# Kernel tuning notes

Hardware: AMD Instinct MI355X
Metric: run time of the kernel (lower is better)

The kernel has to match this reference:

```python
import jax, jax.numpy as jnp
import numpy as np

N_QUBITS = 10
N_LAYERS = 4
DIM = 2 ** N_QUBITS


def _bit(v, q, n):
    return (v >> (n - 1 - q)) & 1


def _cnot_indices(control, target, n):
    idx0, idx1 = [], []
    for i in range(2 ** n):
        if _bit(i, control, n) == 1 and _bit(i, target, n) == 0:
            idx0.append(i)
            idx1.append(i | (1 << (n - 1 - target)))
    return np.asarray(idx0, np.int32), np.asarray(idx1, np.int32)


# static precomputed CNOT swap indices for pairs (q, (q+1) % n)
_CNOT = [_cnot_indices(q, (q + 1) % N_QUBITS, N_QUBITS) for q in range(N_QUBITS)]
# Z expectation masks: [n_qubits, dim] of +/-1
_ZMASK = np.array([[1.0 - 2.0 * _bit(i, q, N_QUBITS) for i in range(DIM)]
                   for q in range(N_QUBITS)], np.float32)


def _rx(t):
    c = jnp.cos(t / 2.0).astype(jnp.complex64)
    s = jnp.sin(t / 2.0).astype(jnp.complex64)
    return jnp.stack([jnp.stack([c, -1j * s], -1),
                      jnp.stack([-1j * s, c], -1)], -2)


def _ry(t):
    c = jnp.cos(t / 2.0).astype(jnp.complex64)
    s = jnp.sin(t / 2.0).astype(jnp.complex64)
    return jnp.stack([jnp.stack([c, -s], -1),
                      jnp.stack([s, c], -1)], -2)


def _rz(t):
    tc = t.astype(jnp.complex64)
    e0 = jnp.exp(-1j * tc / 2.0)
    e1 = jnp.exp(1j * tc / 2.0)
    z = jnp.zeros_like(e0)
    return jnp.stack([jnp.stack([e0, z], -1),
                      jnp.stack([z, e1], -1)], -2)


def _apply_gate(state, gate, q):
    # state: [b, DIM] complex64; gate: [2,2] or [b,2,2]
    b = state.shape[0]
    psi = state.reshape((b,) + (2,) * N_QUBITS)
    psi = jnp.moveaxis(psi, q + 1, N_QUBITS).reshape(b, DIM // 2, 2)
    if gate.ndim == 3:
        out = jnp.einsum('bmi,bij->bmj', psi, gate)
    else:
        out = jnp.einsum('bmi,ij->bmj', psi, gate)
    out = out.reshape((b,) + (2,) * N_QUBITS)
    out = jnp.moveaxis(out, N_QUBITS, q + 1)
    return out.reshape(b, DIM)


def _cnot(state, idx0, idx1):
    return state.at[:, idx0].set(state[:, idx1]).at[:, idx1].set(state[:, idx0])


def setup_inputs() -> dict:
    key = jax.random.key(0)
    k1, k2, k3, k4 = jax.random.split(key, 4)
    x = jax.random.normal(k1, (16384, 3), jnp.float32)
    enc_W = jax.random.normal(k2, (N_QUBITS, 3), jnp.float32) * 0.3
    enc_b = jax.random.normal(k3, (N_QUBITS,), jnp.float32) * 0.1
    theta = jax.random.normal(k4, (N_LAYERS, N_QUBITS, 3), jnp.float32) * 0.04
    return {"x": x, "enc_W": enc_W, "enc_b": enc_b, "theta": theta}


def reference(x, enc_W, enc_b, theta):
    b = x.shape[0]
    enc = jnp.pi * jnp.tanh(x @ enc_W.T + enc_b)  # [b, n_qubits]
    state = jnp.zeros((b, DIM), jnp.complex64).at[:, 0].set(1.0 + 0j)
    # batched encoding RY rotations
    for q in range(N_QUBITS):
        state = _apply_gate(state, _ry(enc[:, q]), q)
    # variational layers (shared gate across batch)
    for layer in range(N_LAYERS):
        for q in range(N_QUBITS):
            state = _apply_gate(state, _rx(theta[layer, q, 0]), q)
            state = _apply_gate(state, _ry(theta[layer, q, 1]), q)
            state = _apply_gate(state, _rz(theta[layer, q, 2]), q)
        for idx0, idx1 in _CNOT:
            state = _cnot(state, idx0, idx1)
    probs = jnp.square(state.real) + jnp.square(state.imag)  # [b, DIM]
    return probs @ jnp.asarray(_ZMASK).T  # [b, n_qubits]
```

## Files before the change

kernel.cpp:

```cpp
#include <hip/hip_runtime.h>
#include <stdint.h>

#define NQ 10
#define NL 4

typedef unsigned int u32;
typedef _Float16 f16x8 __attribute__((ext_vector_type(8)));
typedef float f32x16 __attribute__((ext_vector_type(16)));
typedef u32 u32x4 __attribute__((ext_vector_type(4)));


__device__ __forceinline__ f32x16 mfma16(f16x8 a, f16x8 b, f32x16 c) {
    return __builtin_amdgcn_mfma_f32_32x32x16_f16(a, b, c, 0, 0, 0);
}
__device__ __forceinline__ f32x16 zero16() {
    f32x16 z;
#pragma unroll
    for (int i = 0; i < 16; i++) z[i] = 0.f;
    return z;
}
__device__ __forceinline__ f16x8 negf(f16x8 v) {
    u32x4 u = __builtin_bit_cast(u32x4, v);
#pragma unroll
    for (int i = 0; i < 4; i++) u[i] ^= 0x80008000u;
    return __builtin_bit_cast(f16x8, u);
}
__device__ __forceinline__ u32 pk2(float a, float b) {
    auto h = __builtin_amdgcn_cvt_pkrtz(a, b);
    return __builtin_bit_cast(u32, h);
}
__device__ __forceinline__ u32 mixhl(u32 s, u32 x) {
    return __builtin_amdgcn_perm(s, x, 0x07060100u);
}
__device__ __forceinline__ f16x8 mk8(u32 a, u32 b, u32 c, u32 d) {
    u32x4 v; v[0] = a; v[1] = b; v[2] = c; v[3] = d;
    return __builtin_bit_cast(f16x8, v);
}
template <int MASK>
__device__ __forceinline__ float swz(float v) {
    return __int_as_float(__builtin_amdgcn_ds_swizzle(__float_as_int(v), (MASK << 10) | 0x1F));
}
template <int MASK>
__device__ __forceinline__ u32 swzu(u32 v) {
    return (u32)__builtin_amdgcn_ds_swizzle((int)v, (MASK << 10) | 0x1F);
}
__device__ __forceinline__ void cmulh(float ar, float ai, float br, float bi, float& cr, float& ci) {
    cr = ar * br - ai * bi;
    ci = ar * bi + ai * br;
}

__global__ void tq_prep(const float* __restrict__ theta, uint16_t* __restrict__ frag) {
    __shared__ float g[NL * NQ][8];
    int tt = threadIdx.x;
    if (tt < NL * NQ) {
        float hx = 0.5f * theta[tt * 3 + 0];
        float hy = 0.5f * theta[tt * 3 + 1];
        float hz = 0.5f * theta[tt * 3 + 2];
        float cx = cosf(hx), sx = sinf(hx);
        float cy = cosf(hy), sy = sinf(hy);
        float cz = cosf(hz), sz = sinf(hz);
        float m00r = cx * cy, m00i = -sx * sy;
        float m01r = -cx * sy, m01i = -sx * cy;
        float m10r = cx * sy, m10i = -sx * cy;
        float m11r = cx * cy, m11i = sx * sy;
        float g00r, g00i, g01r, g01i, g10r, g10i, g11r, g11i;
        cmulh(m00r, m00i, cz, -sz, g00r, g00i);
        cmulh(m10r, m10i, cz, -sz, g10r, g10i);
        cmulh(m01r, m01i, cz, sz, g01r, g01i);
        cmulh(m11r, m11i, cz, sz, g11r, g11i);
        g[tt][0] = g00r; g[tt][1] = g00i; g[tt][2] = g01r; g[tt][3] = g01i;
        g[tt][4] = g10r; g[tt][5] = g10i; g[tt][6] = g11r; g[tt][7] = g11i;
    }
    __syncthreads();
    int t = blockIdx.x * blockDim.x + tt;
    int lane = t & 63, kh = (t >> 6) & 1, part = (t >> 7) & 1, mat = (t >> 8) & 1, l = t >> 9;
    int mn = lane & 31, hf = (lane >> 5) & 1;
    int mne = (l < NL - 1) ? ((mn ^ (mn >> 1)) & 31) : mn;
#pragma unroll
    for (int j = 0; j < 8; j++) {
        int k = kh * 16 + ((j >> 2)) * 8 + hf * 4 + (j & 3);
        float pr = 1.f, pi = 0.f;
#pragma unroll
        for (int u = 0; u < 5; u++) {
            int q = mat ? (5 + u) : u;
            int bi_ = (k >> (4 - u)) & 1;
            int bo_ = (mne >> (4 - u)) & 1;
            const float* gg = g[l * NQ + q];
            float er = gg[(bi_ * 2 + bo_) * 2 + 0];
            float ei = gg[(bi_ * 2 + bo_) * 2 + 1];
            float nr, ni;
            cmulh(pr, pi, er, ei, nr, ni);
            pr = nr;
            pi = ni;
        }
        float v = part ? pi : pr;
        _Float16 h = (_Float16)v;
        frag[t * 8 + j] = __builtin_bit_cast(unsigned short, h);
    }
    if (blockIdx.x == 0 && tt < 128) {
        int ln = tt & 63, kh2 = tt >> 6;
        int q = ln & 31, hf2 = (ln >> 5) & 1;
        u32 M = (q == 0) ? 0xFu : (q == 1) ? 0x18u : (q == 2) ? 0x1Cu : (q == 3) ? 0x1Eu : 0x1Fu;
        uint16_t* o = frag + ((32 + kh2) * 64 + ln) * 8;
#pragma unroll
        for (int j = 0; j < 8; j++) {
            int k = kh2 * 16 + ((j >> 2)) * 8 + hf2 * 4 + (j & 3);
            float v = (__builtin_popcount((u32)k & M) & 1) ? -1.f : 1.f;
            _Float16 h = (_Float16)v;
            o[j] = __builtin_bit_cast(unsigned short, h);
        }
    }
}

__global__ __launch_bounds__(256) void tq_main(
    const float* __restrict__ x, const float* __restrict__ encW,
    const float* __restrict__ encb, const uint16_t* __restrict__ frag,
    float* __restrict__ out, int batch) {
    int tid = threadIdx.x;
    int wave = (blockIdx.x * blockDim.x + tid) >> 6;
    int lane = tid & 63;
    if (wave >= batch) return;
    const int col = lane & 31;
    const int half_ = lane >> 5;
    const bool hb = half_ != 0;
    const bool c0 = (lane & 1) != 0;

    float x0 = x[wave * 3 + 0], x1 = x[wave * 3 + 1], x2 = x[wave * 3 + 2];
    float hc = 1.f, hs = 0.f;
    if (lane < NQ) {
        float tta = 3.14159265358979323846f *
                    tanhf(x0 * encW[lane * 3 + 0] + x1 * encW[lane * 3 + 1] +
                          x2 * encW[lane * 3 + 2] + encb[lane]);
        float h = 0.5f * tta;
        hc = cosf(h);
        hs = sinf(h);
    }
    float fcv[NQ], fsv[NQ];
#pragma unroll
    for (int q = 0; q < NQ; q++) {
        fcv[q] = __shfl(hc, q, 64);
        fsv[q] = __shfl(hs, q, 64);
    }
    float colf = 1.f;
    colf *= ((col >> 4) & 1) ? -fsv[5] : fcv[5];
    colf *= ((col >> 3) & 1) ? -fsv[6] : fcv[6];
    colf *= ((col >> 2) & 1) ? -fsv[7] : fcv[7];
    colf *= ((col >> 1) & 1) ? -fsv[8] : fcv[8];
    colf *= (col & 1) ? -fsv[9] : fcv[9];
    float f2h = half_ ? -fsv[2] : fcv[2];
    float gj[8];
#pragma unroll
    for (int j = 0; j < 8; j++) {
        gj[j] = ((j & 4) ? -fsv[1] : fcv[1]) * ((j & 2) ? -fsv[3] : fcv[3]) *
                ((j & 1) ? -fsv[4] : fcv[4]);
    }
    f16x8 Sr0, Sr1, Si0, Si1;
#pragma unroll
    for (int j = 0; j < 8; j++) {
        Sr0[j] = (_Float16)(fcv[0] * f2h * gj[j] * colf);
        Sr1[j] = (_Float16)(-fsv[0] * f2h * gj[j] * colf);
        Si0[j] = (_Float16)0.f;
        Si1[j] = (_Float16)0.f;
    }

    const f16x8* fr = (const f16x8*)frag;
#define FRAG(f) fr[((f)*64) + lane]

    f32x16 Ur, Ui;
#pragma unroll
    for (int l = 0; l < NL; l++) {
        f16x8 Wr0 = FRAG(8 * l + 0), Wr1 = FRAG(8 * l + 1);
        f16x8 Wi0 = FRAG(8 * l + 2), Wi1 = FRAG(8 * l + 3);
        f16x8 Vr0 = FRAG(8 * l + 4), Vr1 = FRAG(8 * l + 5);
        f16x8 Vi0 = FRAG(8 * l + 6), Vi1 = FRAG(8 * l + 7);

        f32x16 Tr = zero16(), Ti = zero16();
        Tr = mfma16(Sr0, Wr0, Tr);
        Tr = mfma16(Sr1, Wr1, Tr);
        Ti = mfma16(Sr0, Wi0, Ti);
        Ti = mfma16(Sr1, Wi1, Ti);
        if (l > 0) {
            f16x8 nSi0 = negf(Si0), nSi1 = negf(Si1);
            Tr = mfma16(nSi0, Wi0, Tr);
            Tr = mfma16(nSi1, Wi1, Tr);
            Ti = mfma16(Si0, Wr0, Ti);
            Ti = mfma16(Si1, Wr1, Ti);
        }

        f16x8 TAr0, TAr1, TAi0, TAi1;
        {
            u32 a0[4], a1[4], b0[4], b1[4];
#pragma unroll
            for (int p = 0; p < 4; p++) {
                a0[p] = pk2(Tr[2 * p], Tr[2 * p + 1]);
                a1[p] = pk2(Tr[8 + 2 * p], Tr[8 + 2 * p + 1]);
                b0[p] = pk2(Ti[2 * p], Ti[2 * p + 1]);
                b1[p] = pk2(Ti[8 + 2 * p], Ti[8 + 2 * p + 1]);
            }
            TAr0 = mk8(a0[0], a0[1], a0[2], a0[3]);
            TAr1 = mk8(a1[0], a1[1], a1[2], a1[3]);
            TAi0 = mk8(b0[0], b0[1], b0[2], b0[3]);
            TAi1 = mk8(b1[0], b1[1], b1[2], b1[3]);
        }

        Ur = zero16();
        Ui = zero16();
        Ur = mfma16(TAr0, Vr0, Ur);
        Ur = mfma16(TAr1, Vr1, Ur);
        {
            f16x8 nTAi0 = negf(TAi0), nTAi1 = negf(TAi1);
            Ur = mfma16(nTAi0, Vi0, Ur);
            Ur = mfma16(nTAi1, Vi1, Ur);
        }
        Ui = mfma16(TAr0, Vi0, Ui);
        Ui = mfma16(TAr1, Vi1, Ui);
        Ui = mfma16(TAi0, Vr0, Ui);
        Ui = mfma16(TAi1, Vr1, Ui);

        if (l < NL - 1) {
            u32 wr0[4], wr1[4], wi0[4], wi1[4];
#pragma unroll
            for (int p = 0; p < 4; p++) {
                wr0[p] = pk2(Ur[2 * p], Ur[2 * p + 1]);
                wr1[p] = pk2(Ur[8 + 2 * p], Ur[8 + 2 * p + 1]);
                wi0[p] = pk2(Ui[2 * p], Ui[2 * p + 1]);
                wi1[p] = pk2(Ui[8 + 2 * p], Ui[8 + 2 * p + 1]);
            }
            u32 s0[4], s1[4], t0[4], t1[4];
#pragma unroll
            for (int p = 0; p < 4; p++) {
                u32 xe0r = c0 ? wr1[p] : wr0[p];
                u32 xe1r = c0 ? wr0[p] : wr1[p];
                u32 xe0i = c0 ? wi1[p] : wi0[p];
                u32 xe1i = c0 ? wi0[p] : wi1[p];
                s0[p] = mixhl(swzu<0x1F>(xe1r), xe0r);
                s1[p] = mixhl(swzu<0x1F>(xe0r), xe1r);
                t0[p] = mixhl(swzu<0x1F>(xe1i), xe0i);
                t1[p] = mixhl(swzu<0x1F>(xe0i), xe1i);
            }
            Sr0 = mk8(s0[0], s0[1], s0[2], s0[3]);
            Sr1 = mk8(s1[0], s1[1], s1[2], s1[3]);
            Si0 = mk8(t0[0], t0[1], t0[2], t0[3]);
            Si1 = mk8(t1[0], t1[1], t1[2], t1[3]);
        }
    }

    f32x16 P;
#pragma unroll
    for (int gi = 0; gi < 16; gi++) P[gi] = Ur[gi] * Ur[gi] + Ui[gi] * Ui[gi];
    f16x8 PB0, PB1;
    {
        u32 p0[4], p1[4];
#pragma unroll
        for (int p = 0; p < 4; p++) {
            p0[p] = pk2(P[2 * p], P[2 * p + 1]);
            p1[p] = pk2(P[8 + 2 * p], P[8 + 2 * p + 1]);
        }
        PB0 = mk8(p0[0], p0[1], p0[2], p0[3]);
        PB1 = mk8(p1[0], p1[1], p1[2], p1[3]);
    }
    f16x8 Srw0 = FRAG(32), Srw1 = FRAG(33);
    f32x16 D = mfma16(Srw0, PB0, mfma16(Srw1, PB1, zero16()));

    u32 b4 = (col >> 4) & 1, b3 = (col >> 3) & 1, b2 = (col >> 2) & 1,
        b1 = (col >> 1) & 1, b0 = col & 1;
    u32 p4 = b4, p43 = p4 ^ b3, p432 = p43 ^ b2, p4321 = p432 ^ b1, pall = p4321 ^ b0;
    u32 sg[6];
    sg[0] = hb ? 0u : pall;
    sg[1] = hb ? p4 : 0u;
    sg[2] = hb ? p43 : 0u;
    sg[3] = hb ? p432 : 0u;
    sg[4] = hb ? 0u : p4321;
    sg[5] = hb ? 0u : pall;
    float red[6];
#pragma unroll
    for (int s = 0; s < 6; s++) {
        float v = __uint_as_float(__float_as_uint(D[s]) ^ (sg[s] << 31));
        v += swz<1>(v);
        v += swz<2>(v);
        v += swz<4>(v);
        v += swz<8>(v);
        v += swz<16>(v);
        red[s] = v;
    }
    int cc = col - ((col >= 4) ? 4 : 0);
    float v = red[0];
    v = (cc == 1) ? red[1] : v;
    v = (cc == 2) ? red[2] : v;
    v = (cc == 3) ? red[3] : v;
    v = (cc == 4) ? red[4] : v;
    v = (cc == 5) ? red[5] : v;
    bool st = hb ? (col >= 4 && col < 8) : (col < 4 || col == 8 || col == 9);
    if (st) out[wave * NQ + col] = v;
}

extern "C" void kernel_launch(void* const* d_in, const int* in_sizes, int n_in,
                              void* d_out, int out_size, void* d_ws, size_t ws_size,
                              hipStream_t stream) {
    const float* x = (const float*)d_in[0];
    const float* encW = (const float*)d_in[1];
    const float* encb = (const float*)d_in[2];
    const float* th = (const float*)d_in[3];
    float* out = (float*)d_out;
    uint16_t* frag = (uint16_t*)d_ws;
    int batch = in_sizes[0] / 3;

    tq_prep<<<2, 1024, 0, stream>>>(th, frag);
    int total_threads = batch * 64;
    tq_main<<<(total_threads + 255) / 256, 256, 0, stream>>>(x, encW, encb, frag, out, batch);
}
```

Before: 98.13 us.

## Fold inter-layer CNOT permutation into extra gate fragments; simplify Z-expectation reduction

The prep kernel now writes extra permuted V-gate fragments (columns XOR 16) for each non-final layer. The main kernel computes both the normal and the permuted output with additional MFMAs, then builds the next-layer operands by direct selection, replacing the ds_swizzle/perm CNOT shuffle. The final reduction swaps the MFMA operand order and uses per-column sign bitmasks plus a single cross-half shuffle, instead of five swizzle-reduction rounds per output. Each of the first three layers gains 8 MFMAs and 4 fragment loads in exchange for removing the cross-lane data movement.

```diff
diff --git a/kernel.cpp b/kernel.cpp
--- a/kernel.cpp
+++ b/kernel.cpp
@@ -29,24 +29,28 @@
     auto h = __builtin_amdgcn_cvt_pkrtz(a, b);
     return __builtin_bit_cast(u32, h);
 }
-__device__ __forceinline__ u32 mixhl(u32 s, u32 x) {
-    return __builtin_amdgcn_perm(s, x, 0x07060100u);
-}
 __device__ __forceinline__ f16x8 mk8(u32 a, u32 b, u32 c, u32 d) {
     u32x4 v; v[0] = a; v[1] = b; v[2] = c; v[3] = d;
     return __builtin_bit_cast(f16x8, v);
 }
-template <int MASK>
-__device__ __forceinline__ float swz(float v) {
-    return __int_as_float(__builtin_amdgcn_ds_swizzle(__float_as_int(v), (MASK << 10) | 0x1F));
-}
-template <int MASK>
-__device__ __forceinline__ u32 swzu(u32 v) {
-    return (u32)__builtin_amdgcn_ds_swizzle((int)v, (MASK << 10) | 0x1F);
-}
-__device__ __forceinline__ void cmulh(float ar, float ai, float br, float bi, float& cr, float& ci) {
-    cr = ar * br - ai * bi;
-    ci = ar * bi + ai * br;
+
+__device__ __forceinline__ float gate_prod(const float g[][8], int l, int mat, int part,
+                                           int k, int mo) {
+    float pr = 1.f, pi = 0.f;
+#pragma unroll
+    for (int u = 0; u < 5; u++) {
+        int q = mat ? (5 + u) : u;
+        int bi_ = (k >> (4 - u)) & 1;
+        int bo_ = (mo >> (4 - u)) & 1;
+        const float* gg = g[l * NQ + q];
+        float er = gg[(bi_ * 2 + bo_) * 2 + 0];
+        float ei = gg[(bi_ * 2 + bo_) * 2 + 1];
+        float nr = pr * er - pi * ei;
+        float ni = pr * ei + pi * er;
+        pr = nr;
+        pi = ni;
+    }
+    return part ? pi : pr;
 }
 
 __global__ void tq_prep(const float* __restrict__ theta, uint16_t* __restrict__ frag) {
@@ -63,11 +67,10 @@
         float m01r = -cx * sy, m01i = -sx * cy;
         float m10r = cx * sy, m10i = -sx * cy;
         float m11r = cx * cy, m11i = sx * sy;
-        float g00r, g00i, g01r, g01i, g10r, g10i, g11r, g11i;
-        cmulh(m00r, m00i, cz, -sz, g00r, g00i);
-        cmulh(m10r, m10i, cz, -sz, g10r, g10i);
-        cmulh(m01r, m01i, cz, sz, g01r, g01i);
-        cmulh(m11r, m11i, cz, sz, g11r, g11i);
+        float g00r = m00r * cz + m00i * sz, g00i = m00i * cz - m00r * sz;
+        float g10r = m10r * cz + m10i * sz, g10i = m10i * cz - m10r * sz;
+        float g01r = m01r * cz - m01i * sz, g01i = m01i * cz + m01r * sz;
+        float g11r = m11r * cz - m11i * sz, g11i = m11i * cz + m11r * sz;
         g[tt][0] = g00r; g[tt][1] = g00i; g[tt][2] = g01r; g[tt][3] = g01i;
         g[tt][4] = g10r; g[tt][5] = g10i; g[tt][6] = g11r; g[tt][7] = g11i;
     }
@@ -79,23 +82,21 @@
 #pragma unroll
     for (int j = 0; j < 8; j++) {
         int k = kh * 16 + ((j >> 2)) * 8 + hf * 4 + (j & 3);
-        float pr = 1.f, pi = 0.f;
-#pragma unroll
-        for (int u = 0; u < 5; u++) {
-            int q = mat ? (5 + u) : u;
-            int bi_ = (k >> (4 - u)) & 1;
-            int bo_ = (mne >> (4 - u)) & 1;
-            const float* gg = g[l * NQ + q];
-            float er = gg[(bi_ * 2 + bo_) * 2 + 0];
-            float ei = gg[(bi_ * 2 + bo_) * 2 + 1];
-            float nr, ni;
-            cmulh(pr, pi, er, ei, nr, ni);
-            pr = nr;
-            pi = ni;
-        }
-        float v = part ? pi : pr;
+        float v = gate_prod(g, l, mat, part, k, mne);
         _Float16 h = (_Float16)v;
         frag[t * 8 + j] = __builtin_bit_cast(unsigned short, h);
+    }
+    if (mat == 1 && l < NL - 1) {
+        int fvf = 34 + l * 4 + part * 2 + kh;
+        int mnf = mne ^ 16;
+        uint16_t* o = frag + ((fvf * 64) + lane) * 8;
+#pragma unroll
+        for (int j = 0; j < 8; j++) {
+            int k = kh * 16 + ((j >> 2)) * 8 + hf * 4 + (j & 3);
+            float v = gate_prod(g, l, 1, part, k, mnf);
+            _Float16 h = (_Float16)v;
+            o[j] = __builtin_bit_cast(unsigned short, h);
+        }
     }
     if (blockIdx.x == 0 && tt < 128) {
         int ln = tt & 63, kh2 = tt >> 6;
@@ -122,7 +123,6 @@
     if (wave >= batch) return;
     const int col = lane & 31;
     const int half_ = lane >> 5;
-    const bool hb = half_ != 0;
     const bool c0 = (lane & 1) != 0;
 
     float x0 = x[wave * 3 + 0], x1 = x[wave * 3 + 1], x2 = x[wave * 3 + 2];
@@ -166,6 +166,8 @@
     const f16x8* fr = (const f16x8*)frag;
 #define FRAG(f) fr[((f)*64) + lane]
 
+    const f32x16 Z = zero16();
+
     f32x16 Ur, Ui;
 #pragma unroll
     for (int l = 0; l < NL; l++) {
@@ -174,10 +176,9 @@
         f16x8 Vr0 = FRAG(8 * l + 4), Vr1 = FRAG(8 * l + 5);
         f16x8 Vi0 = FRAG(8 * l + 6), Vi1 = FRAG(8 * l + 7);
 
-        f32x16 Tr = zero16(), Ti = zero16();
-        Tr = mfma16(Sr0, Wr0, Tr);
+        f32x16 Tr = mfma16(Sr0, Wr0, Z);
         Tr = mfma16(Sr1, Wr1, Tr);
-        Ti = mfma16(Sr0, Wi0, Ti);
+        f32x16 Ti = mfma16(Sr0, Wi0, Z);
         Ti = mfma16(Sr1, Wi1, Ti);
         if (l > 0) {
             f16x8 nSi0 = negf(Si0), nSi1 = negf(Si1);
@@ -202,44 +203,50 @@
             TAi0 = mk8(b0[0], b0[1], b0[2], b0[3]);
             TAi1 = mk8(b1[0], b1[1], b1[2], b1[3]);
         }
-
-        Ur = zero16();
-        Ui = zero16();
-        Ur = mfma16(TAr0, Vr0, Ur);
+        f16x8 nTAi0 = negf(TAi0), nTAi1 = negf(TAi1);
+
+        Ur = mfma16(TAr0, Vr0, Z);
         Ur = mfma16(TAr1, Vr1, Ur);
-        {
-            f16x8 nTAi0 = negf(TAi0), nTAi1 = negf(TAi1);
-            Ur = mfma16(nTAi0, Vi0, Ur);
-            Ur = mfma16(nTAi1, Vi1, Ur);
-        }
-        Ui = mfma16(TAr0, Vi0, Ui);
+        Ur = mfma16(nTAi0, Vi0, Ur);
+        Ur = mfma16(nTAi1, Vi1, Ur);
+        Ui = mfma16(TAr0, Vi0, Z);
         Ui = mfma16(TAr1, Vi1, Ui);
         Ui = mfma16(TAi0, Vr0, Ui);
         Ui = mfma16(TAi1, Vr1, Ui);
 
         if (l < NL - 1) {
-            u32 wr0[4], wr1[4], wi0[4], wi1[4];
+            f16x8 Vfr0 = FRAG(34 + l * 4 + 0), Vfr1 = FRAG(34 + l * 4 + 1);
+            f16x8 Vfi0 = FRAG(34 + l * 4 + 2), Vfi1 = FRAG(34 + l * 4 + 3);
+
+            f32x16 Urf = mfma16(TAr0, Vfr0, Z);
+            Urf = mfma16(TAr1, Vfr1, Urf);
+            Urf = mfma16(nTAi0, Vfi0, Urf);
+            Urf = mfma16(nTAi1, Vfi1, Urf);
+
+            u32 s0[4], s1[4];
 #pragma unroll
             for (int p = 0; p < 4; p++) {
-                wr0[p] = pk2(Ur[2 * p], Ur[2 * p + 1]);
-                wr1[p] = pk2(Ur[8 + 2 * p], Ur[8 + 2 * p + 1]);
-                wi0[p] = pk2(Ui[2 * p], Ui[2 * p + 1]);
-                wi1[p] = pk2(Ui[8 + 2 * p], Ui[8 + 2 * p + 1]);
-            }
-            u32 s0[4], s1[4], t0[4], t1[4];
-#pragma unroll
-            for (int p = 0; p < 4; p++) {
-                u32 xe0r = c0 ? wr1[p] : wr0[p];
-                u32 xe1r = c0 ? wr0[p] : wr1[p];
-                u32 xe0i = c0 ? wi1[p] : wi0[p];
-                u32 xe1i = c0 ? wi0[p] : wi1[p];
-                s0[p] = mixhl(swzu<0x1F>(xe1r), xe0r);
-                s1[p] = mixhl(swzu<0x1F>(xe0r), xe1r);
-                t0[p] = mixhl(swzu<0x1F>(xe1i), xe0i);
-                t1[p] = mixhl(swzu<0x1F>(xe0i), xe1i);
+                s0[p] = pk2(c0 ? Ur[2 * p + 8] : Ur[2 * p],
+                            c0 ? Urf[2 * p + 9] : Urf[2 * p + 1]);
+                s1[p] = pk2(c0 ? Ur[2 * p] : Ur[2 * p + 8],
+                            c0 ? Urf[2 * p + 1] : Urf[2 * p + 9]);
             }
             Sr0 = mk8(s0[0], s0[1], s0[2], s0[3]);
             Sr1 = mk8(s1[0], s1[1], s1[2], s1[3]);
+
+            f32x16 Uif = mfma16(TAr0, Vfi0, Z);
+            Uif = mfma16(TAr1, Vfi1, Uif);
+            Uif = mfma16(TAi0, Vfr0, Uif);
+            Uif = mfma16(TAi1, Vfr1, Uif);
+
+            u32 t0[4], t1[4];
+#pragma unroll
+            for (int p = 0; p < 4; p++) {
+                t0[p] = pk2(c0 ? Ui[2 * p + 8] : Ui[2 * p],
+                            c0 ? Uif[2 * p + 9] : Uif[2 * p + 1]);
+                t1[p] = pk2(c0 ? Ui[2 * p] : Ui[2 * p + 8],
+                            c0 ? Uif[2 * p + 1] : Uif[2 * p + 9]);
+            }
             Si0 = mk8(t0[0], t0[1], t0[2], t0[3]);
             Si1 = mk8(t1[0], t1[1], t1[2], t1[3]);
         }
@@ -260,38 +267,26 @@
         PB1 = mk8(p1[0], p1[1], p1[2], p1[3]);
     }
     f16x8 Srw0 = FRAG(32), Srw1 = FRAG(33);
-    f32x16 D = mfma16(Srw0, PB0, mfma16(Srw1, PB1, zero16()));
-
-    u32 b4 = (col >> 4) & 1, b3 = (col >> 3) & 1, b2 = (col >> 2) & 1,
-        b1 = (col >> 1) & 1, b0 = col & 1;
-    u32 p4 = b4, p43 = p4 ^ b3, p432 = p43 ^ b2, p4321 = p432 ^ b1, pall = p4321 ^ b0;
-    u32 sg[6];
-    sg[0] = hb ? 0u : pall;
-    sg[1] = hb ? p4 : 0u;
-    sg[2] = hb ? p43 : 0u;
-    sg[3] = hb ? p432 : 0u;
-    sg[4] = hb ? 0u : p4321;
-    sg[5] = hb ? 0u : pall;
-    float red[6];
-#pragma unroll
-    for (int s = 0; s < 6; s++) {
-        float v = __uint_as_float(__float_as_uint(D[s]) ^ (sg[s] << 31));
-        v += swz<1>(v);
-        v += swz<2>(v);
-        v += swz<4>(v);
-        v += swz<8>(v);
-        v += swz<16>(v);
-        red[s] = v;
-    }
-    int cc = col - ((col >= 4) ? 4 : 0);
-    float v = red[0];
-    v = (cc == 1) ? red[1] : v;
-    v = (cc == 2) ? red[2] : v;
-    v = (cc == 3) ? red[3] : v;
-    v = (cc == 4) ? red[4] : v;
-    v = (cc == 5) ? red[5] : v;
-    bool st = hb ? (col >= 4 && col < 8) : (col < 4 || col == 8 || col == 9);
-    if (st) out[wave * NQ + col] = v;
+    f32x16 E = mfma16(PB0, Srw0, mfma16(PB1, Srw1, Z));
+
+    u32 SM = (col == 0 || col == 9) ? 0x96696996u
+             : (col == 5)           ? 0xFFFF0000u
+             : (col == 6)           ? 0x00FFFF00u
+             : (col == 7)           ? 0xF00F0FF0u
+             : (col == 8)           ? 0x3CC3C33Cu
+                                    : 0u;
+    u32 SMh = SM >> (half_ * 4);
+    float acc0 = 0.f, acc1 = 0.f;
+#pragma unroll
+    for (int i = 0; i < 16; i++) {
+        const int ci = (i & 3) + 8 * (i >> 2);
+        u32 m = (SMh << (31 - ci)) & 0x80000000u;
+        float v = __uint_as_float(__float_as_uint(E[i]) ^ m);
+        if (i & 1) acc1 += v; else acc0 += v;
+    }
+    float acc = acc0 + acc1;
+    float tot = acc + __shfl(acc, lane ^ 32, 64);
+    if (lane < NQ) out[wave * NQ + lane] = tot;
 }
 
 extern "C" void kernel_launch(void* const* d_in, const int* in_sizes, int n_in,
@@ -305,7 +300,7 @@
     uint16_t* frag = (uint16_t*)d_ws;
     int batch = in_sizes[0] / 3;
 
-    tq_prep<<<2, 1024, 0, stream>>>(th, frag);
+    tq_prep<<<8, 256, 0, stream>>>(th, frag);
     int total_threads = batch * 64;
     tq_main<<<(total_threads + 255) / 256, 256, 0, stream>>>(x, encW, encb, frag, out, batch);
 }
```

After: 190.5 us. 1.94x slower.
